# Optimization experiments

Measured on AMD Instinct MI355X. Metric: run time of the kernel, lower is better.

Reference implementation:

```python
import jax, jax.numpy as jnp
import numpy as np

N_NODES = 50000
N_EDGES = 800000
NFEATS = 256
HFEATS = 256
N_TARGET = 8
NEG_SLOPE = 0.2


def setup_inputs() -> dict:
    key = jax.random.key(0)
    ks = jax.random.split(key, 16)
    s = 1.0 / np.sqrt(HFEATS)
    inp = {
        'hv': jax.random.normal(ks[0], (N_NODES, NFEATS), dtype=jnp.float32),
        'src': jax.random.randint(ks[1], (N_EDGES,), 0, N_NODES, dtype=jnp.int32),
        'dst': jax.random.randint(ks[2], (N_EDGES,), 0, N_NODES, dtype=jnp.int32),
        'W_in': jax.random.normal(ks[3], (NFEATS, HFEATS), dtype=jnp.float32) * (1.0 / np.sqrt(NFEATS)),
        'b_in': jnp.zeros((HFEATS,), dtype=jnp.float32),
        'W_ro': jax.random.normal(ks[4], (3 * HFEATS, N_TARGET), dtype=jnp.float32) * (1.0 / np.sqrt(3 * HFEATS)),
        'b_ro': jnp.zeros((N_TARGET,), dtype=jnp.float32),
    }
    for i in range(1, 4):
        k = jax.random.split(ks[4 + i], 4)
        inp[f'fc{i}'] = jax.random.normal(k[0], (HFEATS, HFEATS), dtype=jnp.float32) * s
        inp[f'al{i}'] = jax.random.normal(k[1], (HFEATS,), dtype=jnp.float32) * s
        inp[f'ar{i}'] = jax.random.normal(k[2], (HFEATS,), dtype=jnp.float32) * s
        inp[f'bias{i}'] = jnp.zeros((HFEATS,), dtype=jnp.float32)
    return inp


def _gat(h, src, dst, fc, al, ar, bias):
    # DGL GATConv, 1 head: fc proj, additive attention, edge softmax over dst, sum agg.
    feat = h @ fc                                  # [N, H]
    el = feat @ al                                 # [N]
    er = feat @ ar                                 # [N]
    e = jax.nn.leaky_relu(el[src] + er[dst], NEG_SLOPE)   # [E]
    m = jax.ops.segment_max(e, dst, num_segments=N_NODES)
    ex = jnp.exp(e - m[dst])
    denom = jax.ops.segment_sum(ex, dst, num_segments=N_NODES)
    a = ex / denom[dst]                            # [E]
    out = jax.ops.segment_sum(feat[src] * a[:, None], dst, num_segments=N_NODES)
    return out + bias


def reference(hv, src, dst, W_in, b_in, W_ro, b_ro,
              fc1, al1, ar1, bias1, fc2, al2, ar2, bias2, fc3, al3, ar3, bias3):
    h0 = hv @ W_in + b_in
    h1 = _gat(jax.nn.relu(h0), src, dst, fc1, al1, ar1, bias1)
    h2 = _gat(jax.nn.relu(h1), src, dst, fc2, al2, ar2, bias2)
    h3 = _gat(jax.nn.relu(h2), src, dst, fc3, al3, ar3, bias3)
    out = jnp.concatenate([h1, h2, h3], axis=-1) @ W_ro + b_ro
    return jax.nn.sigmoid(out)
```

## Files before the change

### kernel.cpp

```cpp
#include <hip/hip_runtime.h>
#include <hip/hip_bf16.h>
#include <math.h>

#define NNODES 50000
#define NEDGES 800000
#define HF 256
#define NEG_SLOPE 0.2f
#define NB 196
#define APAD 12288

typedef short bf16x8 __attribute__((ext_vector_type(8)));
typedef float f32x4 __attribute__((ext_vector_type(4)));
typedef float f32x2 __attribute__((ext_vector_type(2)));

__device__ __forceinline__ unsigned short f2bf(float f) {
  unsigned u = __float_as_uint(f);
  unsigned r = u + 0x7FFFu + ((u >> 16) & 1u);
  return (unsigned short)(r >> 16);
}
__device__ __forceinline__ float bf2f(unsigned short u) {
  return __uint_as_float((unsigned)u << 16);
}
__device__ __forceinline__ uint2 pack4(const float* v) {
  uint2 r;
  r.x = (unsigned)f2bf(v[0]) | ((unsigned)f2bf(v[1]) << 16);
  r.y = (unsigned)f2bf(v[2]) | ((unsigned)f2bf(v[3]) << 16);
  return r;
}
__device__ __forceinline__ uint4 pack8(const float* v) {
  uint4 r;
  r.x = (unsigned)f2bf(v[0]) | ((unsigned)f2bf(v[1]) << 16);
  r.y = (unsigned)f2bf(v[2]) | ((unsigned)f2bf(v[3]) << 16);
  r.z = (unsigned)f2bf(v[4]) | ((unsigned)f2bf(v[5]) << 16);
  r.w = (unsigned)f2bf(v[6]) | ((unsigned)f2bf(v[7]) << 16);
  return r;
}

__device__ __forceinline__ int permc(int p) {
  return (p & 192) | ((p & 3) << 4) | ((p & 63) >> 2);
}

#define GLOAD_LDS16(gsrc, ldst)                                                \
  __builtin_amdgcn_global_load_lds(                                           \
      (const __attribute__((address_space(1))) unsigned int*)(const void*)(gsrc), \
      (__attribute__((address_space(3))) unsigned int*)(void*)(ldst), 16, 0, 0)

__device__ __forceinline__ void slot_decode(int s, int& row, int& kb) {
  row = ((s >> 3) << 1) | (((s >> 2) & 1) ^ ((s >> 4) & 1));
  kb  = ((s & 1) ^ (row & 1)) | ((((s >> 1) & 1) ^ ((s >> 3) & 1)) << 1);
}

__global__ __launch_bounds__(256)
void conv_hv(const float* __restrict__ x, unsigned short* __restrict__ o) {
  size_t i = (size_t)(blockIdx.x * 256 + threadIdx.x) * 8;
  float4 a = *(const float4*)(x + i);
  float4 b = *(const float4*)(x + i + 4);
  float v[8] = {a.x, a.y, a.z, a.w, b.x, b.y, b.z, b.w};
  *(uint4*)(o + i) = pack8(v);
}

__global__ __launch_bounds__(256)
void conv_wt(const float* __restrict__ W0, const float* __restrict__ W1,
             const float* __restrict__ W2, const float* __restrict__ W3,
             unsigned short* __restrict__ WT) {
  int mat = blockIdx.y;
  const float* W = mat == 0 ? W0 : (mat == 1 ? W1 : (mat == 2 ? W2 : W3));
  int i = blockIdx.x * 256 + threadIdx.x;
  int n = i >> 8, p = i & 255;
  int k = (mat == 0) ? p : permc(p);
  WT[(size_t)mat * 65536 + i] = f2bf(W[(size_t)k * 256 + n]);
}

__global__ __launch_bounds__(256)
void conv_wro(const float* __restrict__ Wro, unsigned short* __restrict__ WroT) {
  int i = blockIdx.x * 256 + threadIdx.x;
  if (i >= 16 * 768) return;
  int n = i / 768, kk = i % 768;
  int part = kk >> 8, q = kk & 255;
  float v = (n < 8) ? Wro[(size_t)((part << 8) + permc(q)) * 8 + n] : 0.f;
  WroT[i] = f2bf(v);
}

template<bool BIAS_RELU, bool DOTS>
__global__ __launch_bounds__(256)
void gemm_bf16(const unsigned short* __restrict__ A, const unsigned short* __restrict__ WT,
               const float* __restrict__ bias,
               const float* __restrict__ al, const float* __restrict__ ar,
               void* __restrict__ Cv,
               float* __restrict__ el, float* __restrict__ er, int M) {
  __shared__ unsigned short As[2][64 * 32];
  __shared__ unsigned short Bs[2][256 * 32];
  __shared__ float sEl[64][4], sEr[64][4];
  const int t = threadIdx.x;
  const int lane = t & 63;
  const int w = t >> 6;
  const int wc = w * 64;
  const int brow = blockIdx.x * 64;

  f32x4 acc[4][4];
#pragma unroll
  for (int i = 0; i < 4; i++)
#pragma unroll
    for (int j = 0; j < 4; j++) acc[i][j] = (f32x4)(0.f);

  int rA, kA;
  slot_decode(w * 64 + lane, rA, kA);
  const unsigned short* aP = A + (size_t)(brow + rA) * 256 + kA * 8;
  const unsigned short* bP[4];
#pragma unroll
  for (int i = 0; i < 4; i++) {
    int rB, kB;
    slot_decode(w * 256 + i * 64 + lane, rB, kB);
    bP[i] = WT + (size_t)rB * 256 + kB * 8;
  }
  unsigned short* lA[2] = {&As[0][w * 512], &As[1][w * 512]};
  unsigned short* lB[2] = {&Bs[0][w * 2048], &Bs[1][w * 2048]};

#define STAGE(buf, kt)                                                         \
  do {                                                                         \
    GLOAD_LDS16(aP + (kt) * 32, lA[buf]);                                      \
    GLOAD_LDS16(bP[0] + (kt) * 32, lB[buf]);                                   \
    GLOAD_LDS16(bP[1] + (kt) * 32, lB[buf] + 512);                             \
    GLOAD_LDS16(bP[2] + (kt) * 32, lB[buf] + 1024);                            \
    GLOAD_LDS16(bP[3] + (kt) * 32, lB[buf] + 1536);                            \
  } while (0)

  const int fr = lane & 15, fq = lane >> 4;
  int ard[4], brd[4];
#pragma unroll
  for (int i = 0; i < 4; i++) {
    int rowA = i * 16 + fr;
    ard[i] = ((rowA * 64 + fq * 16) ^ ((rowA & 7) << 4));
    int rowB = wc + i * 16 + fr;
    brd[i] = ((rowB * 64 + fq * 16) ^ ((rowB & 7) << 4));
  }

  STAGE(0, 0);
  __syncthreads();
  int cur = 0;
#pragma unroll
  for (int kt = 0; kt < 8; kt++) {
    if (kt < 7) STAGE(cur ^ 1, kt + 1);
    bf16x8 af[4], bfr[4];
#pragma unroll
    for (int i = 0; i < 4; i++) {
      af[i]  = *(const bf16x8*)((const char*)As[cur] + ard[i]);
      bfr[i] = *(const bf16x8*)((const char*)Bs[cur] + brd[i]);
    }
#pragma unroll
    for (int i = 0; i < 4; i++)
#pragma unroll
      for (int j = 0; j < 4; j++)
        acc[i][j] = __builtin_amdgcn_mfma_f32_16x16x32_bf16(af[i], bfr[j], acc[i][j], 0, 0, 0);
    if (kt < 7) {
      __syncthreads();
      cur ^= 1;
    }
  }
#undef STAGE

#pragma unroll
  for (int i = 0; i < 4; i++) {
#pragma unroll
    for (int r = 0; r < 4; r++) {
      int row = brow + i * 16 + fq * 4 + r;
      if (row < M) {
        float v[4];
#pragma unroll
        for (int j = 0; j < 4; j++) {
          float x = acc[i][j][r];
          if (BIAS_RELU) x = fmaxf(x + bias[wc + j * 16 + fr], 0.f);
          v[j] = x;
        }
        if constexpr (DOTS) {
          int pk = __builtin_amdgcn_cvt_pk_fp8_f32(v[0], v[1], 0, false);
          pk = __builtin_amdgcn_cvt_pk_fp8_f32(v[2], v[3], pk, true);
          *(unsigned*)((unsigned char*)Cv + (size_t)row * 256 + wc + fr * 4) = (unsigned)pk;
        } else {
          *(uint2*)((unsigned short*)Cv + (size_t)row * 256 + wc + fr * 4) = pack4(v);
        }
      }
    }
  }

  if constexpr (DOTS) {
    float alv[4], arv[4];
#pragma unroll
    for (int j = 0; j < 4; j++) {
      int colj = wc + j * 16 + fr;
      alv[j] = al[colj];
      arv[j] = ar[colj];
    }
    float pel[16], per_[16];
#pragma unroll
    for (int i = 0; i < 4; i++)
#pragma unroll
      for (int r = 0; r < 4; r++) {
        float se = 0.f, sr = 0.f;
#pragma unroll
        for (int j = 0; j < 4; j++) {
          se = fmaf(acc[i][j][r], alv[j], se);
          sr = fmaf(acc[i][j][r], arv[j], sr);
        }
        pel[i * 4 + r] = se;
        per_[i * 4 + r] = sr;
      }
#pragma unroll
    for (int off = 1; off < 16; off <<= 1)
#pragma unroll
      for (int k = 0; k < 16; k++) {
        pel[k] += __shfl_xor(pel[k], off);
        per_[k] += __shfl_xor(per_[k], off);
      }
    if (fr == 0) {
#pragma unroll
      for (int i = 0; i < 4; i++)
#pragma unroll
        for (int r = 0; r < 4; r++) {
          int rl = i * 16 + fq * 4 + r;
          sEl[rl][w] = pel[i * 4 + r];
          sEr[rl][w] = per_[i * 4 + r];
        }
    }
    __syncthreads();
    if (t < 64) {
      int row = brow + t;
      if (row < M) {
        el[row] = sEl[t][0] + sEl[t][1] + sEl[t][2] + sEl[t][3];
        er[row] = sEr[t][0] + sEr[t][1] + sEr[t][2] + sEr[t][3];
      }
    }
  }
}

__global__ __launch_bounds__(256)
void hist_dst(const int* __restrict__ dst, int* __restrict__ cnt) {
  int e = blockIdx.x * 256 + threadIdx.x;
  if (e < NEDGES) atomicAdd(&cnt[dst[e]], 1);
}

__global__ __launch_bounds__(256)
void block_sums(const int* __restrict__ cnt, int* __restrict__ bsum) {
  __shared__ int sm[256];
  int t = threadIdx.x;
  int i = blockIdx.x * 256 + t;
  sm[t] = (i < NNODES) ? cnt[i] : 0;
  __syncthreads();
  for (int off = 128; off; off >>= 1) {
    if (t < off) sm[t] += sm[t + off];
    __syncthreads();
  }
  if (t == 0) bsum[blockIdx.x] = sm[0];
}

__global__ __launch_bounds__(256)
void scan_bsums(const int* __restrict__ bsum, int* __restrict__ boff) {
  __shared__ int sm[256];
  int t = threadIdx.x;
  sm[t] = (t < NB) ? bsum[t] : 0;
  __syncthreads();
  for (int off = 1; off < 256; off <<= 1) {
    int v = (t >= off) ? sm[t - off] : 0;
    __syncthreads();
    sm[t] += v;
    __syncthreads();
  }
  if (t < NB) boff[t] = (t == 0) ? 0 : sm[t - 1];
}

__global__ __launch_bounds__(256)
void write_rowptr(const int* __restrict__ cnt, const int* __restrict__ boff,
                  int* __restrict__ rowptr, int* __restrict__ woff) {
  __shared__ int sm[256];
  int t = threadIdx.x;
  int i = blockIdx.x * 256 + t;
  int v = (i < NNODES) ? cnt[i] : 0;
  sm[t] = v;
  __syncthreads();
  for (int off = 1; off < 256; off <<= 1) {
    int x = (t >= off) ? sm[t - off] : 0;
    __syncthreads();
    sm[t] += x;
    __syncthreads();
  }
  int excl = boff[blockIdx.x] + sm[t] - v;
  if (i < NNODES) { rowptr[i] = excl; woff[i] = excl; }
  if (i == NNODES - 1) rowptr[NNODES] = excl + v;
}

__global__ __launch_bounds__(256)
void scatter_csr(const int* __restrict__ src, const int* __restrict__ dst,
                 int* __restrict__ woff, int* __restrict__ col) {
  int e = blockIdx.x * 256 + threadIdx.x;
  if (e >= NEDGES) return;
  int d = dst[e];
  int p = atomicAdd(&woff[d], 1);
  col[p] = src[e];
}

template<bool WRITE_RELU>
__global__ __launch_bounds__(256)
void gat_csr(const int* __restrict__ rowptr, const int* __restrict__ col,
             const float* __restrict__ el, const float* __restrict__ er,
             const unsigned char* __restrict__ feat8, const float* __restrict__ bias,
             unsigned short* __restrict__ h, unsigned short* __restrict__ hrelu) {
  int d = blockIdx.x * 4 + (threadIdx.x >> 6);
  int lane = threadIdx.x & 63;
  if (d >= NNODES) return;
  const int start = rowptr[d], end = rowptr[d + 1];
  float bv[4];
#pragma unroll
  for (int m = 0; m < 4; m++)
    bv[m] = bias[((lane >> 4) << 6) | (m << 4) | (lane & 15)];
  const size_t obase = (size_t)d * HF + lane * 4;
  if (start == end) {
    *(uint2*)(h + obase) = pack4(bv);
    if (WRITE_RELU) {
      float rv[4] = {fmaxf(bv[0], 0.f), fmaxf(bv[1], 0.f), fmaxf(bv[2], 0.f), fmaxf(bv[3], 0.f)};
      *(uint2*)(hrelu + obase) = pack4(rv);
    }
    return;
  }
  const float erd = er[d];

  float sm = 0.f;
  f32x2 acl = (f32x2)(0.f), ach = (f32x2)(0.f);

  for (int c0 = start; c0 < end; c0 += 64) {
    int j = c0 + lane;
    float ex = 0.f;
    int s = 0;
    if (j < end) {
      s = col[j];
      float x = el[s] + erd;
      x = x > 0.f ? x : NEG_SLOPE * x;
      ex = __expf(x);
    }
    sm += ex;
    int n = min(64, end - c0);
    for (int q = 0; q < n; q += 8) {
      int su[8];
      float eu[8];
#pragma unroll
      for (int u = 0; u < 8; u++) {
        su[u] = __builtin_amdgcn_readlane(s, q + u);
        eu[u] = __uint_as_float(
            (unsigned)__builtin_amdgcn_readlane((int)__float_as_uint(ex), q + u));
      }
      unsigned fv[8];
#pragma unroll
      for (int u = 0; u < 8; u++)
        fv[u] = *(const unsigned*)(feat8 + (size_t)su[u] * 256 + lane * 4);
#pragma unroll
      for (int u = 0; u < 8; u++) {
        f32x2 lo = __builtin_amdgcn_cvt_pk_f32_fp8((int)fv[u], false);
        f32x2 hi = __builtin_amdgcn_cvt_pk_f32_fp8((int)fv[u], true);
        f32x2 ev = {eu[u], eu[u]};
        acl = lo * ev + acl;
        ach = hi * ev + ach;
      }
    }
  }
#pragma unroll
  for (int off = 32; off; off >>= 1) sm += __shfl_xor(sm, off);

  const float rcp = 1.f / sm;
  float ov[4];
  ov[0] = fmaf(acl.x, rcp, bv[0]);
  ov[1] = fmaf(acl.y, rcp, bv[1]);
  ov[2] = fmaf(ach.x, rcp, bv[2]);
  ov[3] = fmaf(ach.y, rcp, bv[3]);
  *(uint2*)(h + obase) = pack4(ov);
  if (WRITE_RELU) {
    float rv[4] = {fmaxf(ov[0], 0.f), fmaxf(ov[1], 0.f), fmaxf(ov[2], 0.f), fmaxf(ov[3], 0.f)};
    *(uint2*)(hrelu + obase) = pack4(rv);
  }
}

__global__ __launch_bounds__(256)
void readout(const unsigned short* __restrict__ h1, const unsigned short* __restrict__ h2,
             const unsigned short* __restrict__ h3, const unsigned short* __restrict__ WroT,
             const float* __restrict__ bro, float* __restrict__ out) {
  const int t = threadIdx.x;
  const int lane = t & 63;
  const int w = t >> 6;
  const int fr = lane & 15, fq = lane >> 4;
  const int r0 = blockIdx.x * 64 + w * 16;
  if (r0 >= NNODES) return;
  const unsigned short* hs[3] = {h1, h2, h3};

  f32x4 acc = (f32x4)(0.f);
  const int koff = fq * 8;
#pragma unroll
  for (int part = 0; part < 3; ++part) {
    const unsigned short* hp = hs[part] + (size_t)(r0 + fr) * HF + koff;
    const unsigned short* wp = WroT + fr * 768 + part * 256 + koff;
#pragma unroll
    for (int kb = 0; kb < 8; ++kb) {
      bf16x8 af = *(const bf16x8*)(hp + kb * 32);
      bf16x8 bf = *(const bf16x8*)(wp + kb * 32);
      acc = __builtin_amdgcn_mfma_f32_16x16x32_bf16(af, bf, acc, 0, 0, 0);
    }
  }
  if (fr < 8) {
    const float b = bro[fr];
#pragma unroll
    for (int r = 0; r < 4; ++r) {
      int row = r0 + fq * 4 + r;
      float v = acc[r] + b;
      out[(size_t)row * 8 + fr] = 1.f / (1.f + expf(-v));
    }
  }
}

extern "C" void kernel_launch(void* const* d_in, const int* in_sizes, int n_in,
                              void* d_out, int out_size, void* d_ws, size_t ws_size,
                              hipStream_t stream) {
  const float* hv   = (const float*)d_in[0];
  const int*   src  = (const int*)d_in[1];
  const int*   dst  = (const int*)d_in[2];
  const float* W_in = (const float*)d_in[3];
  const float* b_in = (const float*)d_in[4];
  const float* W_ro = (const float*)d_in[5];
  const float* b_ro = (const float*)d_in[6];
  const float* fc[3]   = {(const float*)d_in[7],  (const float*)d_in[11], (const float*)d_in[15]};
  const float* al[3]   = {(const float*)d_in[8],  (const float*)d_in[12], (const float*)d_in[16]};
  const float* ar[3]   = {(const float*)d_in[9],  (const float*)d_in[13], (const float*)d_in[17]};
  const float* bias[3] = {(const float*)d_in[10], (const float*)d_in[14], (const float*)d_in[18]};
  float* out = (float*)d_out;

  const size_t NH = (size_t)NNODES * HF;
  unsigned short* h1    = (unsigned short*)d_ws;
  unsigned short* h2    = h1 + NH;
  unsigned short* h3    = h2 + NH;
  unsigned char*  feat8 = (unsigned char*)(h3 + NH);
  unsigned short* hrelu = (unsigned short*)(feat8 + NH);
  unsigned short* hvbf  = hrelu + NH + APAD;
  float* el   = (float*)(hvbf + NH + APAD);
  float* er   = el + NNODES;
  int* rowptr = (int*)(er + NNODES);
  int* woff   = rowptr + NNODES + 1;
  int* cnt    = woff + NNODES;
  int* bsum   = cnt + NNODES;
  int* boff   = bsum + 256;
  int* col    = boff + 256;
  unsigned short* WT = (unsigned short*)(col + NEDGES);
  unsigned short* WroT = WT + 4 * 65536;

  const int gemm_grid = (NNODES + 63) / 64;
  const int ep_grid = (NEDGES + 255) / 256;
  const int gat_grid = (NNODES + 3) / 4;
  const int ro_grid = (NNODES + 63) / 64;

  conv_hv<<<(int)(NH / 2048), 256, 0, stream>>>(hv, hvbf);
  conv_wt<<<dim3(256, 4), 256, 0, stream>>>(W_in, fc[0], fc[1], fc[2], WT);
  conv_wro<<<48, 256, 0, stream>>>(W_ro, WroT);

  hipMemsetAsync(cnt, 0, NNODES * sizeof(int), stream);
  hist_dst<<<ep_grid, 256, 0, stream>>>(dst, cnt);
  block_sums<<<NB, 256, 0, stream>>>(cnt, bsum);
  scan_bsums<<<1, 256, 0, stream>>>(bsum, boff);
  write_rowptr<<<NB, 256, 0, stream>>>(cnt, boff, rowptr, woff);
  scatter_csr<<<ep_grid, 256, 0, stream>>>(src, dst, woff, col);

  gemm_bf16<true, false><<<gemm_grid, 256, 0, stream>>>(
      hvbf, WT, b_in, nullptr, nullptr, hrelu, nullptr, nullptr, NNODES);

  unsigned short* houts[3] = {h1, h2, h3};
  for (int l = 0; l < 3; ++l) {
    unsigned short* hl = houts[l];
    gemm_bf16<false, true><<<gemm_grid, 256, 0, stream>>>(
        hrelu, WT + (size_t)(l + 1) * 65536, nullptr, al[l], ar[l], feat8, el, er, NNODES);
    if (l < 2)
      gat_csr<true><<<gat_grid, 256, 0, stream>>>(rowptr, col, el, er, feat8, bias[l], hl, hrelu);
    else
      gat_csr<false><<<gat_grid, 256, 0, stream>>>(rowptr, col, el, er, feat8, bias[l], hl, hrelu);
  }

  readout<<<ro_grid, 256, 0, stream>>>(h1, h2, h3, WroT, b_ro, out);
}
```

Measured before the change: 349.2 us.

## Build CSR via two-pass bucket sort with shared-memory atomics

Replaces the global-atomic histogram and scatter CSR build with a two-level bucket sort. A coarse pass histograms and scatters edges into 196 buckets of 256 destination nodes using LDS atomics. A fine pass per bucket then computes per-node offsets and writes the col array. This removes the memset and the heavy contention from global atomics on random addresses, at the cost of an extra pass through an 8-byte edge buffer and more workspace.

```diff
diff --git a/kernel.cpp b/kernel.cpp
--- a/kernel.cpp
+++ b/kernel.cpp
@@ -6,8 +6,10 @@
 #define NEDGES 800000
 #define HF 256
 #define NEG_SLOPE 0.2f
-#define NB 196
 #define APAD 12288
+#define CHUNK 3125
+#define NBUCK 196
+#define NG (NBUCK * 256)
 
 typedef short bf16x8 __attribute__((ext_vector_type(8)));
 typedef float f32x4 __attribute__((ext_vector_type(4)));
@@ -234,68 +236,111 @@
 }
 
 __global__ __launch_bounds__(256)
-void hist_dst(const int* __restrict__ dst, int* __restrict__ cnt) {
-  int e = blockIdx.x * 256 + threadIdx.x;
-  if (e < NEDGES) atomicAdd(&cnt[dst[e]], 1);
-}
-
-__global__ __launch_bounds__(256)
-void block_sums(const int* __restrict__ cnt, int* __restrict__ bsum) {
+void hist_coarse(const int* __restrict__ dst, int* __restrict__ gh) {
+  __shared__ int lh[NBUCK];
+  const int t = threadIdx.x, blk = blockIdx.x;
+  if (t < NBUCK) lh[t] = 0;
+  __syncthreads();
+  const int base = blk * CHUNK;
+  for (int i = t; i < CHUNK; i += 256)
+    atomicAdd(&lh[dst[base + i] >> 8], 1);
+  __syncthreads();
+  if (t < NBUCK) gh[t * 256 + blk] = lh[t];
+}
+
+__global__ __launch_bounds__(256)
+void bsum2(const int* __restrict__ g, int* __restrict__ bsum) {
+  __shared__ int sm[256];
+  int t = threadIdx.x;
+  sm[t] = g[blockIdx.x * 256 + t];
+  __syncthreads();
+  for (int off = 128; off; off >>= 1) {
+    if (t < off) sm[t] += sm[t + off];
+    __syncthreads();
+  }
+  if (t == 0) bsum[blockIdx.x] = sm[0];
+}
+
+__global__ __launch_bounds__(256)
+void sscan2(const int* __restrict__ bsum, int* __restrict__ boff) {
+  __shared__ int sm[256];
+  int t = threadIdx.x;
+  sm[t] = (t < NBUCK) ? bsum[t] : 0;
+  __syncthreads();
+  for (int o = 1; o < 256; o <<= 1) {
+    int v = (t >= o) ? sm[t - o] : 0;
+    __syncthreads();
+    sm[t] += v;
+    __syncthreads();
+  }
+  if (t < NBUCK) boff[t] = (t == 0) ? 0 : sm[t - 1];
+}
+
+__global__ __launch_bounds__(256)
+void abase2(const int* __restrict__ g, const int* __restrict__ boff,
+            int* __restrict__ abase) {
   __shared__ int sm[256];
   int t = threadIdx.x;
   int i = blockIdx.x * 256 + t;
-  sm[t] = (i < NNODES) ? cnt[i] : 0;
-  __syncthreads();
-  for (int off = 128; off; off >>= 1) {
-    if (t < off) sm[t] += sm[t + off];
-    __syncthreads();
-  }
-  if (t == 0) bsum[blockIdx.x] = sm[0];
-}
-
-__global__ __launch_bounds__(256)
-void scan_bsums(const int* __restrict__ bsum, int* __restrict__ boff) {
-  __shared__ int sm[256];
-  int t = threadIdx.x;
-  sm[t] = (t < NB) ? bsum[t] : 0;
-  __syncthreads();
-  for (int off = 1; off < 256; off <<= 1) {
-    int v = (t >= off) ? sm[t - off] : 0;
-    __syncthreads();
-    sm[t] += v;
-    __syncthreads();
-  }
-  if (t < NB) boff[t] = (t == 0) ? 0 : sm[t - 1];
-}
-
-__global__ __launch_bounds__(256)
-void write_rowptr(const int* __restrict__ cnt, const int* __restrict__ boff,
-                  int* __restrict__ rowptr, int* __restrict__ woff) {
-  __shared__ int sm[256];
-  int t = threadIdx.x;
-  int i = blockIdx.x * 256 + t;
-  int v = (i < NNODES) ? cnt[i] : 0;
+  int v = g[i];
   sm[t] = v;
   __syncthreads();
-  for (int off = 1; off < 256; off <<= 1) {
-    int x = (t >= off) ? sm[t - off] : 0;
+  for (int o = 1; o < 256; o <<= 1) {
+    int x = (t >= o) ? sm[t - o] : 0;
     __syncthreads();
     sm[t] += x;
     __syncthreads();
   }
-  int excl = boff[blockIdx.x] + sm[t] - v;
-  if (i < NNODES) { rowptr[i] = excl; woff[i] = excl; }
-  if (i == NNODES - 1) rowptr[NNODES] = excl + v;
-}
-
-__global__ __launch_bounds__(256)
-void scatter_csr(const int* __restrict__ src, const int* __restrict__ dst,
-                 int* __restrict__ woff, int* __restrict__ col) {
-  int e = blockIdx.x * 256 + threadIdx.x;
-  if (e >= NEDGES) return;
-  int d = dst[e];
-  int p = atomicAdd(&woff[d], 1);
-  col[p] = src[e];
+  abase[i] = boff[blockIdx.x] + sm[t] - v;
+}
+
+__global__ __launch_bounds__(256)
+void scatter_coarse(const int* __restrict__ src, const int* __restrict__ dst,
+                    const int* __restrict__ abase, uint2* __restrict__ ebuf) {
+  __shared__ int off[NBUCK];
+  const int t = threadIdx.x, blk = blockIdx.x;
+  if (t < NBUCK) off[t] = abase[t * 256 + blk];
+  __syncthreads();
+  const int base = blk * CHUNK;
+  for (int i = t; i < CHUNK; i += 256) {
+    int e = base + i;
+    int d = dst[e], s = src[e];
+    int p = atomicAdd(&off[d >> 8], 1);
+    ebuf[p] = make_uint2((unsigned)s, (unsigned)d);
+  }
+}
+
+__global__ __launch_bounds__(256)
+void fine_sort(const uint2* __restrict__ ebuf, const int* __restrict__ abase,
+               int* __restrict__ rowptr, int* __restrict__ col) {
+  __shared__ int hist[256], pre[256], off[256];
+  const int t = threadIdx.x, b = blockIdx.x;
+  const int bstart = abase[b * 256];
+  const int bend = (b < NBUCK - 1) ? abase[(b + 1) * 256] : NEDGES;
+  hist[t] = 0;
+  __syncthreads();
+  for (int e = bstart + t; e < bend; e += 256)
+    atomicAdd(&hist[ebuf[e].y & 255], 1);
+  __syncthreads();
+  pre[t] = hist[t];
+  __syncthreads();
+  for (int o = 1; o < 256; o <<= 1) {
+    int v = (t >= o) ? pre[t - o] : 0;
+    __syncthreads();
+    pre[t] += v;
+    __syncthreads();
+  }
+  const int excl = bstart + pre[t] - hist[t];
+  const int node = b * 256 + t;
+  if (node < NNODES) rowptr[node] = excl;
+  if (node == NNODES - 1) rowptr[NNODES] = NEDGES;
+  off[t] = excl;
+  __syncthreads();
+  for (int e = bstart + t; e < bend; e += 256) {
+    uint2 ed = ebuf[e];
+    int p = atomicAdd(&off[ed.y & 255], 1);
+    col[p] = (int)ed.x;
+  }
 }
 
 template<bool WRITE_RELU>
@@ -439,16 +484,16 @@
   float* el   = (float*)(hvbf + NH + APAD);
   float* er   = el + NNODES;
   int* rowptr = (int*)(er + NNODES);
-  int* woff   = rowptr + NNODES + 1;
-  int* cnt    = woff + NNODES;
-  int* bsum   = cnt + NNODES;
+  int* gh     = rowptr + NNODES + 1;
+  int* abase  = gh + NG;
+  int* bsum   = abase + NG;
   int* boff   = bsum + 256;
   int* col    = boff + 256;
-  unsigned short* WT = (unsigned short*)(col + NEDGES);
+  uint2* ebuf = (uint2*)(col + NEDGES);
+  unsigned short* WT = (unsigned short*)(ebuf + NEDGES);
   unsigned short* WroT = WT + 4 * 65536;
 
   const int gemm_grid = (NNODES + 63) / 64;
-  const int ep_grid = (NEDGES + 255) / 256;
   const int gat_grid = (NNODES + 3) / 4;
   const int ro_grid = (NNODES + 63) / 64;
 
@@ -456,12 +501,12 @@
   conv_wt<<<dim3(256, 4), 256, 0, stream>>>(W_in, fc[0], fc[1], fc[2], WT);
   conv_wro<<<48, 256, 0, stream>>>(W_ro, WroT);
 
-  hipMemsetAsync(cnt, 0, NNODES * sizeof(int), stream);
-  hist_dst<<<ep_grid, 256, 0, stream>>>(dst, cnt);
-  block_sums<<<NB, 256, 0, stream>>>(cnt, bsum);
-  scan_bsums<<<1, 256, 0, stream>>>(bsum, boff);
-  write_rowptr<<<NB, 256, 0, stream>>>(cnt, boff, rowptr, woff);
-  scatter_csr<<<ep_grid, 256, 0, stream>>>(src, dst, woff, col);
+  hist_coarse<<<256, 256, 0, stream>>>(dst, gh);
+  bsum2<<<NBUCK, 256, 0, stream>>>(gh, bsum);
+  sscan2<<<1, 256, 0, stream>>>(bsum, boff);
+  abase2<<<NBUCK, 256, 0, stream>>>(gh, boff, abase);
+  scatter_coarse<<<256, 256, 0, stream>>>(src, dst, abase, ebuf);
+  fine_sort<<<NBUCK, 256, 0, stream>>>(ebuf, abase, rowptr, col);
 
   gemm_bf16<true, false><<<gemm_grid, 256, 0, stream>>>(
       hvbf, WT, b_in, nullptr, nullptr, hrelu, nullptr, nullptr, NNODES);
```

Measured after the change: 279.6 us. -19.9%, faster.
